# Optimization experiments

Hardware: AMD Instinct MI355X
Metric: run time of the kernel (lower is better)

The kernel has to match this reference:

```python
import jax, jax.numpy as jnp
import numpy as np

COS_EPS = 1e-6
LN_EPS = 1e-5

def _cosine_sim(a, b):
    # PyTorch F.cosine_similarity(dim=1, eps): dot / (max(||a||,eps)*max(||b||,eps))
    dot = jnp.sum(a * b, axis=1)
    na = jnp.maximum(jnp.linalg.norm(a, axis=1), COS_EPS)
    nb = jnp.maximum(jnp.linalg.norm(b, axis=1), COS_EPS)
    return dot / (na * nb)

def _layer_norm(x, gamma, beta):
    mu = jnp.mean(x, axis=-1, keepdims=True)
    var = jnp.mean(jnp.square(x - mu), axis=-1, keepdims=True)
    return (x - mu) * jax.lax.rsqrt(var + LN_EPS) * gamma + beta

def setup_inputs() -> dict:
    B, I, H = 8192, 1024, 1024
    key = jax.random.key(0)
    ks = jax.random.split(key, 10)
    s_in = 1.0 / np.sqrt(I + H)
    s_im = 1.0 / np.sqrt(I)
    return {
        "x": jax.random.normal(ks[0], (B, I), jnp.float32),
        "hx": jax.random.normal(ks[1], (B, H), jnp.float32),
        "cx": jax.random.normal(ks[2], (B, H), jnp.float32),
        # main gate linear: [I+H, 4H]
        "W": jax.random.uniform(ks[3], (I + H, 4 * H), jnp.float32, -s_in, s_in),
        "b": jax.random.uniform(ks[4], (4 * H,), jnp.float32, -s_in, s_in),
        # input_mapped: [I, H]
        "Wm": jax.random.uniform(ks[5], (I, H), jnp.float32, -s_im, s_im),
        "bm": jax.random.uniform(ks[6], (H,), jnp.float32, -s_im, s_im),
        # 4 LayerNorms (i, f, g, o)
        "gammas": 1.0 + 0.1 * jax.random.normal(ks[7], (4, H), jnp.float32),
        "betas": 0.1 * jax.random.normal(ks[8], (4, H), jnp.float32),
    }

def reference(x, hx, cx, W, b, Wm, bm, gammas, betas):
    H = hx.shape[1]
    # cosine attention gate between mapped input and hidden state
    input_mapped = x @ Wm + bm                                   # [B, H]
    attn = jax.nn.sigmoid(_cosine_sim(input_mapped, hx))[:, None]  # [B, 1]
    x_mod = x + attn * x
    gates = jnp.concatenate([x_mod, hx], axis=1) @ W + b         # [B, 4H]
    i_g, f_g, g_g, o_g = jnp.split(gates, 4, axis=1)
    i_g = jax.nn.sigmoid(_layer_norm(i_g, gammas[0], betas[0]))
    f_g = jax.nn.sigmoid(_layer_norm(f_g, gammas[1], betas[1]))
    g_g = jnp.tanh(_layer_norm(g_g, gammas[2], betas[2]))
    o_g = jax.nn.sigmoid(_layer_norm(o_g, gammas[3], betas[3]))
    cx_new = f_g * cx + i_g * g_g
    hx_new = o_g * jnp.tanh(cx_new)
    gate_co = jax.nn.sigmoid((_cosine_sim(hx_new, cx_new)[:, None] + 1.0) / 2.0)
    hx_modulated = hx_new + hx_new * gate_co
    return (hx_modulated, cx_new)
```

## Files before the change

### kernel.cpp

```cpp
#include <hip/hip_runtime.h>
#include <hip/hip_bf16.h>

#define DEV __device__ __forceinline__

typedef unsigned short u16;
typedef unsigned int u32;
typedef __attribute__((ext_vector_type(8))) short bf16x8;
typedef __attribute__((ext_vector_type(4))) float f32x4;

DEV float bf2f(u16 v) { u32 u = ((u32)v) << 16; return __builtin_bit_cast(float, u); }
DEV u16 f2bf(float f) {
    u32 u = __builtin_bit_cast(u32, f);
    u32 r = (u + 0x7fffu + ((u >> 16) & 1u)) >> 16;
    return (u16)r;
}
DEV float lo16(u32 u) { return __builtin_bit_cast(float, u << 16); }
DEV float hi16(u32 u) { return __builtin_bit_cast(float, u & 0xffff0000u); }
DEV float sigm(float x) { return 1.f / (1.f + __expf(-x)); }
DEV float clamp4(float v) { return fminf(fmaxf(v, -1e4f), 1e4f); }
DEV float loadf(const void* p, size_t i, int isf) {
    return isf ? clamp4(((const float*)p)[i]) : clamp4(bf2f(((const u16*)p)[i]));
}
DEV void load8(const void* p, size_t off, int isf, float* o) {
    if (isf) {
        const float* s = (const float*)p + off;
#pragma unroll
        for (int e = 0; e < 8; ++e) o[e] = clamp4(s[e]);
    } else {
        uint4 q = *(const uint4*)((const u16*)p + off);
        o[0] = clamp4(lo16(q.x)); o[1] = clamp4(hi16(q.x));
        o[2] = clamp4(lo16(q.y)); o[3] = clamp4(hi16(q.y));
        o[4] = clamp4(lo16(q.z)); o[5] = clamp4(hi16(q.z));
        o[6] = clamp4(lo16(q.w)); o[7] = clamp4(hi16(q.w));
    }
}
DEV uint4 pack8(const float* a) {
    uint4 q;
    q.x = (u32)f2bf(a[0]) | ((u32)f2bf(a[1]) << 16);
    q.y = (u32)f2bf(a[2]) | ((u32)f2bf(a[3]) << 16);
    q.z = (u32)f2bf(a[4]) | ((u32)f2bf(a[5]) << 16);
    q.w = (u32)f2bf(a[6]) | ((u32)f2bf(a[7]) << 16);
    return q;
}
DEV void store8(void* p, size_t off, int isf, const float* a) {
    if (isf) {
        float* d = (float*)p + off;
        *(float4*)(d) = (float4){a[0], a[1], a[2], a[3]};
        *(float4*)(d + 4) = (float4){a[4], a[5], a[6], a[7]};
    } else {
        *(uint4*)((u16*)p + off) = pack8(a);
    }
}

DEV void gload16(const void* g, void* l) {
    __builtin_amdgcn_global_load_lds(
        (const __attribute__((address_space(1))) void*)g,
        (__attribute__((address_space(3))) void*)l, 16, 0, 0);
}

__global__ void detect_dtype(const u32* __restrict__ xw, u32* __restrict__ flag) {
    const int lane = threadIdx.x & 63;
    int cnt = 0;
    for (int k = 0; k < 32; ++k) {
        u32 e = (xw[lane + 64 * k] >> 7) & 0xff;
        cnt += (e >= 118 && e <= 130) ? 1 : 0;
    }
#pragma unroll
    for (int off = 32; off > 0; off >>= 1) cnt += __shfl_xor(cnt, off, 64);
    if (lane == 0) *flag = (cnt > 1024) ? 0u : 1u;
}

__global__ __launch_bounds__(256) void cvt2_bf16(
    const void* __restrict__ sa, const void* __restrict__ sb,
    u16* __restrict__ da, u16* __restrict__ db, int n8each,
    const u32* __restrict__ flagp) {
    const int isf = (int)*flagp;
    if (!isf) return;
    int i = blockIdx.x * 256 + threadIdx.x;
    const void* s; u16* d; int j;
    if (i < n8each) { s = sa; d = da; j = i; }
    else            { s = sb; d = db; j = i - n8each; }
    size_t off = (size_t)j * 8;
    float a[8];
    load8(s, off, 1, a);
    *(uint4*)(d + off) = pack8(a);
}

__global__ __launch_bounds__(256) void tr_any(const void* __restrict__ src,
                                              u16* __restrict__ dst,
                                              int R, int C,
                                              const u32* __restrict__ flagp) {
    const int isf = (int)*flagp;
    __shared__ __align__(16) u16 t[32][33];
    int tx = threadIdx.x & 31, ty = threadIdx.x >> 5;
    int c0 = blockIdx.x * 32, r0 = blockIdx.y * 32;
#pragma unroll
    for (int i = 0; i < 32; i += 8)
        t[ty + i][tx] = f2bf(loadf(src, (size_t)(r0 + ty + i) * C + (c0 + tx), isf));
    __syncthreads();
#pragma unroll
    for (int i = 0; i < 32; i += 8)
        dst[(size_t)(c0 + ty + i) * R + (r0 + tx)] = t[tx][ty + i];
}

__global__ __launch_bounds__(512, 2) void gemm256(
    const u16* __restrict__ A0c, const void* __restrict__ A0r,
    const u16* __restrict__ A1c, const void* __restrict__ A1r, int K0,
    const u16* __restrict__ Bt, const void* __restrict__ bias,
    const u32* __restrict__ flagp,
    u16* __restrict__ Cout, int M, int N, int K) {
    const int isf = (int)*flagp;
    const u16* const A0 = isf ? A0c : (const u16*)A0r;
    const u16* const A1 = isf ? A1c : (const u16*)A1r;
    __shared__ __align__(16) u16 lds[65536];
    u16* const ldsA = lds;
    u16* const ldsB = lds + 32768;
    const int tid = threadIdx.x;
    const int wave = tid >> 6, lane = tid & 63;
    const int wm = wave >> 2, wn = wave & 3;

    int bx = blockIdx.x, by = blockIdx.y;
    {
        const int gx = gridDim.x;
        const int nwg = gx * gridDim.y;
        if ((nwg & 7) == 0) {
            int lid = by * gx + bx;
            int swz = (lid & 7) * (nwg >> 3) + (lid >> 3);
            bx = swz % gx; by = swz / gx;
        }
    }
    const int m0 = by * 256, n0 = bx * 256;
    const int NT = K >> 6;

    size_t qA[2][2], qB[2][2];
#pragma unroll
    for (int h = 0; h < 2; ++h)
#pragma unroll
        for (int c = 0; c < 2; ++c) {
            int p = h * 16384 + c * 8192 + wave * 1024 + lane * 16;
            int lg = p ^ (((p >> 9) & 1) << 5);
            int s = lg >> 10, lr = (lg >> 6) & 15;
            int k = ((s & 1) << 5) + ((lg & 63) >> 1);
            int m = ((s >> 3) & 1) * 128 + ((s >> 4) & 1) * 64 +
                    ((s >> 1) & 3) * 16 + lr;
            qA[h][c] = (size_t)(m0 + m) * (size_t)K0 + (size_t)k;
            int ns = ((s >> 2) & 3) * 64 + ((s >> 4) & 1) * 32 +
                     ((s >> 1) & 1) * 16 + lr;
            int gn = (ns & ~63) | ((ns & 15) * 4 + ((ns >> 4) & 3));
            qB[h][c] = (size_t)(n0 + gn) * (size_t)K + (size_t)k;
        }

    const int mrow = lane & 15;
    const int kfr = (lane >> 4) * 8;
    const int aSwz = (mrow * 32 + kfr) ^ ((mrow & 8) << 1);

    f32x4 acc[8][4];
#pragma unroll
    for (int i = 0; i < 8; ++i)
#pragma unroll
        for (int j = 0; j < 4; ++j) acc[i][j] = (f32x4){0.f, 0.f, 0.f, 0.f};

#define ASEG(kt, AS_, KK_) const u16* AS_; int KK_; \
    if ((kt) < K0) { AS_ = A0; KK_ = (kt); } else { AS_ = A1; KK_ = (kt) - K0; }

    {
        ASEG(0, As0, kk0);
        gload16(As0 + qA[0][0] + kk0, ldsA + wave * 512);
        gload16(As0 + qA[0][1] + kk0, ldsA + 4096 + wave * 512);
        gload16(Bt + qB[1][0], ldsB + 8192 + wave * 512);
        gload16(Bt + qB[1][1], ldsB + 8192 + 4096 + wave * 512);
        gload16(As0 + qA[1][0] + kk0, ldsA + 8192 + wave * 512);
        gload16(As0 + qA[1][1] + kk0, ldsA + 8192 + 4096 + wave * 512);
        gload16(Bt + qB[0][0], ldsB + wave * 512);
        gload16(Bt + qB[0][1], ldsB + 4096 + wave * 512);
        if (NT > 1) {
            ASEG(64, As1, kk1);
            gload16(As1 + qA[0][0] + kk1, ldsA + 16384 + wave * 512);
            gload16(As1 + qA[0][1] + kk1, ldsA + 16384 + 4096 + wave * 512);
            gload16(Bt + qB[1][0] + 64, ldsB + 16384 + 8192 + wave * 512);
            gload16(Bt + qB[1][1] + 64, ldsB + 16384 + 8192 + 4096 + wave * 512);
            gload16(As1 + qA[1][0] + kk1, ldsA + 16384 + 8192 + wave * 512);
            gload16(As1 + qA[1][1] + kk1, ldsA + 16384 + 8192 + 4096 + wave * 512);
            asm volatile("s_waitcnt vmcnt(6)" ::: "memory");
        } else {
            asm volatile("s_waitcnt vmcnt(0)" ::: "memory");
        }
        __builtin_amdgcn_s_barrier();
    }

    bf16x8 af0[4][2], af1[4][2], bfA[2][2], bfB[2][2];
    {
        const u16* ab = &ldsA[(wm * 8) * 512];
#pragma unroll
        for (int mt2 = 0; mt2 < 4; ++mt2)
#pragma unroll
            for (int ks = 0; ks < 2; ++ks)
                af0[mt2][ks] = *(const bf16x8*)&ab[(mt2 * 2 + ks) * 512 + aSwz];
        const u16* bb = &ldsB[(wn * 4) * 512];
#pragma unroll
        for (int nt2 = 0; nt2 < 2; ++nt2)
#pragma unroll
            for (int ks = 0; ks < 2; ++ks)
                bfA[nt2][ks] = *(const bf16x8*)&bb[(nt2 * 2 + ks) * 512 + aSwz];
    }

    for (int t = 0; t < NT; ++t) {
        const int bufb = (t & 1) << 14;
        const int obufb = bufb ^ 16384;
        const int k0 = t << 6;

        {
            const u16* ab = &ldsA[bufb + (16 + wm * 8) * 512];
#pragma unroll
            for (int mt2 = 0; mt2 < 4; ++mt2)
#pragma unroll
                for (int ks = 0; ks < 2; ++ks)
                    af1[mt2][ks] = *(const bf16x8*)&ab[(mt2 * 2 + ks) * 512 + aSwz];
        }
        if (t + 1 < NT) {
            gload16(Bt + qB[0][0] + (k0 + 64), ldsB + obufb + wave * 512);
            gload16(Bt + qB[0][1] + (k0 + 64), ldsB + obufb + 4096 + wave * 512);
        }
        __builtin_amdgcn_s_barrier();
        __builtin_amdgcn_s_setprio(1);
#pragma unroll
        for (int mt2 = 0; mt2 < 4; ++mt2)
#pragma unroll
            for (int nt2 = 0; nt2 < 2; ++nt2)
#pragma unroll
                for (int ks = 0; ks < 2; ++ks)
                    acc[mt2][nt2] = __builtin_amdgcn_mfma_f32_16x16x32_bf16(
                        af0[mt2][ks], bfA[nt2][ks], acc[mt2][nt2], 0, 0, 0);
        __builtin_amdgcn_s_setprio(0);

        {
            const u16* bb = &ldsB[bufb + (16 + wn * 4) * 512];
#pragma unroll
            for (int nt2 = 0; nt2 < 2; ++nt2)
#pragma unroll
                for (int ks = 0; ks < 2; ++ks)
                    bfB[nt2][ks] = *(const bf16x8*)&bb[(nt2 * 2 + ks) * 512 + aSwz];
        }
        __builtin_amdgcn_s_barrier();
        if (t + 2 < NT) {
            ASEG(k0 + 128, As2, kk2);
            gload16(As2 + qA[0][0] + kk2, ldsA + bufb + wave * 512);
            gload16(As2 + qA[0][1] + kk2, ldsA + bufb + 4096 + wave * 512);
        }
        __builtin_amdgcn_s_setprio(1);
#pragma unroll
        for (int mt2 = 0; mt2 < 4; ++mt2)
#pragma unroll
            for (int nt2 = 0; nt2 < 2; ++nt2)
#pragma unroll
                for (int ks = 0; ks < 2; ++ks)
                    acc[4 + mt2][nt2] = __builtin_amdgcn_mfma_f32_16x16x32_bf16(
                        af1[mt2][ks], bfA[nt2][ks], acc[4 + mt2][nt2], 0, 0, 0);
#pragma unroll
        for (int mt2 = 0; mt2 < 4; ++mt2)
#pragma unroll
            for (int nt2 = 0; nt2 < 2; ++nt2)
#pragma unroll
                for (int ks = 0; ks < 2; ++ks)
                    acc[mt2][2 + nt2] = __builtin_amdgcn_mfma_f32_16x16x32_bf16(
                        af0[mt2][ks], bfB[nt2][ks], acc[mt2][2 + nt2], 0, 0, 0);
        __builtin_amdgcn_s_setprio(0);

        __builtin_amdgcn_s_barrier();
        if (t + 2 < NT) {
            gload16(Bt + qB[1][0] + (k0 + 128), ldsB + bufb + 8192 + wave * 512);
            gload16(Bt + qB[1][1] + (k0 + 128), ldsB + bufb + 8192 + 4096 + wave * 512);
            ASEG(k0 + 128, As3, kk3);
            gload16(As3 + qA[1][0] + kk3, ldsA + bufb + 8192 + wave * 512);
            gload16(As3 + qA[1][1] + kk3, ldsA + bufb + 8192 + 4096 + wave * 512);
            asm volatile("s_waitcnt vmcnt(6)" ::: "memory");
        } else {
            asm volatile("s_waitcnt vmcnt(0)" ::: "memory");
        }
        __builtin_amdgcn_s_barrier();
        if (t + 1 < NT) {
            const u16* ab = &ldsA[obufb + (wm * 8) * 512];
#pragma unroll
            for (int mt2 = 0; mt2 < 4; ++mt2)
#pragma unroll
                for (int ks = 0; ks < 2; ++ks)
                    af0[mt2][ks] = *(const bf16x8*)&ab[(mt2 * 2 + ks) * 512 + aSwz];
            const u16* bb = &ldsB[obufb + (wn * 4) * 512];
#pragma unroll
            for (int nt2 = 0; nt2 < 2; ++nt2)
#pragma unroll
                for (int ks = 0; ks < 2; ++ks)
                    bfA[nt2][ks] = *(const bf16x8*)&bb[(nt2 * 2 + ks) * 512 + aSwz];
        }
        __builtin_amdgcn_s_setprio(1);
#pragma unroll
        for (int mt2 = 0; mt2 < 4; ++mt2)
#pragma unroll
            for (int nt2 = 0; nt2 < 2; ++nt2)
#pragma unroll
                for (int ks = 0; ks < 2; ++ks)
                    acc[4 + mt2][2 + nt2] = __builtin_amdgcn_mfma_f32_16x16x32_bf16(
                        af1[mt2][ks], bfB[nt2][ks], acc[4 + mt2][2 + nt2], 0, 0, 0);
        __builtin_amdgcn_s_setprio(0);
    }
#undef ASEG

    const int q = lane >> 4;
    const int cbase = n0 + wn * 64 + mrow * 4;
    float bv[4];
#pragma unroll
    for (int tt = 0; tt < 4; ++tt) bv[tt] = loadf(bias, cbase + tt, isf);
#pragma unroll
    for (int mt = 0; mt < 8; ++mt) {
        int row0 = m0 + wm * 128 + mt * 16 + q * 4;
#pragma unroll
        for (int r = 0; r < 4; ++r) {
            uint2 pk;
            pk.x = (u32)f2bf(acc[mt][0][r] + bv[0]) |
                   ((u32)f2bf(acc[mt][1][r] + bv[1]) << 16);
            pk.y = (u32)f2bf(acc[mt][2][r] + bv[2]) |
                   ((u32)f2bf(acc[mt][3][r] + bv[3]) << 16);
            *(uint2*)(Cout + (size_t)(row0 + r) * N + cbase) = pk;
        }
    }
}

__global__ __launch_bounds__(256) void attn_xmod(
    const u16* __restrict__ im,
    const u16* __restrict__ hxc, const void* __restrict__ hxr,
    const u16* __restrict__ xc, const void* __restrict__ xr,
    const u32* __restrict__ flagp, u16* __restrict__ xmod) {
    const int isf = (int)*flagp;
    const u16* hx = isf ? hxc : (const u16*)hxr;
    const u16* x = isf ? xc : (const u16*)xr;
    const int lane = threadIdx.x & 63;
    const int row = blockIdx.x * 4 + (threadIdx.x >> 6);
    float dot = 0.f, na = 0.f, nb = 0.f;
#pragma unroll
    for (int j = 0; j < 2; ++j) {
        size_t off = (size_t)row * 1024 + lane * 8 + j * 512;
        float a[8], h[8];
        load8(im, off, 0, a);
        load8(hx, off, 0, h);
#pragma unroll
        for (int e = 0; e < 8; ++e) {
            dot += a[e] * h[e]; na += a[e] * a[e]; nb += h[e] * h[e];
        }
    }
#pragma unroll
    for (int off = 32; off > 0; off >>= 1) {
        dot += __shfl_xor(dot, off, 64);
        na += __shfl_xor(na, off, 64);
        nb += __shfl_xor(nb, off, 64);
    }
    float cs = dot / (fmaxf(sqrtf(na), 1e-6f) * fmaxf(sqrtf(nb), 1e-6f));
    float fac = 1.f + sigm(cs);
#pragma unroll
    for (int j = 0; j < 2; ++j) {
        size_t off = (size_t)row * 1024 + lane * 8 + j * 512;
        float a[8];
        load8(x, off, 0, a);
#pragma unroll
        for (int e = 0; e < 8; ++e) a[e] *= fac;
        *(uint4*)(xmod + off) = pack8(a);
    }
}

__global__ __launch_bounds__(256) void ln_lstm(
    const u16* __restrict__ gates, const void* __restrict__ cx,
    const void* __restrict__ gammas, const void* __restrict__ betas,
    const u32* __restrict__ flagp, void* __restrict__ out, int BH) {
    const int isf = (int)*flagp;
    const int lane = threadIdx.x & 63;
    const int row = blockIdx.x * 4 + (threadIdx.x >> 6);
    float v[4][16];
    float s[4] = {0.f, 0.f, 0.f, 0.f}, ss[4] = {0.f, 0.f, 0.f, 0.f};
#pragma unroll
    for (int c = 0; c < 4; ++c) {
#pragma unroll
        for (int j = 0; j < 2; ++j) {
            size_t off = (size_t)row * 4096 + c * 1024 + lane * 8 + j * 512;
            float* vp = &v[c][j * 8];
            load8(gates, off, 0, vp);
#pragma unroll
            for (int e = 0; e < 8; ++e) { s[c] += vp[e]; ss[c] += vp[e] * vp[e]; }
        }
    }
#pragma unroll
    for (int off = 32; off > 0; off >>= 1) {
#pragma unroll
        for (int c = 0; c < 4; ++c) {
            s[c] += __shfl_xor(s[c], off, 64);
            ss[c] += __shfl_xor(ss[c], off, 64);
        }
    }
    float mean[4], rstd[4];
#pragma unroll
    for (int c = 0; c < 4; ++c) {
        mean[c] = s[c] * (1.f / 1024.f);
        float var = ss[c] * (1.f / 1024.f) - mean[c] * mean[c];
        rstd[c] = rsqrtf(fmaxf(var, 0.f) + 1e-5f);
    }
#pragma unroll
    for (int c = 0; c < 4; ++c) {
#pragma unroll
        for (int j = 0; j < 2; ++j) {
            size_t off = (size_t)(c * 1024 + lane * 8 + j * 512);
            float g[8], bb[8];
            load8(gammas, off, isf, g);
            load8(betas, off, isf, bb);
            float* vp = &v[c][j * 8];
#pragma unroll
            for (int e = 0; e < 8; ++e) {
                float y = (vp[e] - mean[c]) * rstd[c] * g[e] + bb[e];
                vp[e] = (c == 2) ? tanhf(y) : sigm(y);
            }
        }
    }
    float hn[16], cn[16];
    float dot = 0.f, nh = 0.f, nc = 0.f;
#pragma unroll
    for (int j = 0; j < 2; ++j) {
        size_t off = (size_t)row * 1024 + lane * 8 + j * 512;
        float cv[8];
        load8(cx, off, isf, cv);
#pragma unroll
        for (int e = 0; e < 8; ++e) {
            int idx = j * 8 + e;
            float c_new = v[1][idx] * cv[e] + v[0][idx] * v[2][idx];
            float h_new = v[3][idx] * tanhf(c_new);
            cn[idx] = c_new; hn[idx] = h_new;
            dot += h_new * c_new; nh += h_new * h_new; nc += c_new * c_new;
        }
    }
#pragma unroll
    for (int off = 32; off > 0; off >>= 1) {
        dot += __shfl_xor(dot, off, 64);
        nh += __shfl_xor(nh, off, 64);
        nc += __shfl_xor(nc, off, 64);
    }
    float cs = dot / (fmaxf(sqrtf(nh), 1e-6f) * fmaxf(sqrtf(nc), 1e-6f));
    float fac = 1.f + sigm((cs + 1.f) * 0.5f);
#pragma unroll
    for (int j = 0; j < 2; ++j) {
        size_t off = (size_t)row * 1024 + lane * 8 + j * 512;
        float ho[8];
#pragma unroll
        for (int e = 0; e < 8; ++e) ho[e] = hn[j * 8 + e] * fac;
        store8(out, off, isf, ho);
        store8(out, (size_t)BH + off, isf, &cn[j * 8]);
    }
}

__global__ void diag_k(u32* __restrict__ out, int ws_ok, int sizes_ok) {
    const int lane = threadIdx.x & 63;
    int mrow = lane & 15, quad = lane >> 4;
    bf16x8 af, bfr;
#pragma unroll
    for (int j = 0; j < 8; ++j) {
        int k = quad * 8 + j;
        af[j] = (short)f2bf((float)(((mrow * 7 + k * 3) % 11) - 5));
        bfr[j] = (short)f2bf((float)(((mrow * 5 + k * 2) % 13) - 6));
    }
    f32x4 cacc = (f32x4){0.f, 0.f, 0.f, 0.f};
    cacc = __builtin_amdgcn_mfma_f32_16x16x32_bf16(af, bfr, cacc, 0, 0, 0);
    int bad = 0;
#pragma unroll
    for (int r = 0; r < 4; ++r) {
        int mr = quad * 4 + r;
        float expv = 0.f;
        for (int k = 0; k < 32; ++k)
            expv += (float)(((mr * 7 + k * 3) % 11) - 5) *
                    (float)(((mrow * 5 + k * 2) % 13) - 6);
        if (fabsf(cacc[r] - expv) > 0.5f) bad = 1;
    }
    int mfma_bad = (__ballot(bad) != 0ull) ? 1 : 0;
    if (lane == 0) {
        if (!sizes_ok)     out[0] = __builtin_bit_cast(u32, 65536.f);
        else if (!ws_ok)   out[0] = __builtin_bit_cast(u32, 131072.f);
        else if (mfma_bad) out[0] = __builtin_bit_cast(u32, 32768.f);
    }
}

extern "C" void kernel_launch(void* const* d_in, const int* in_sizes, int n_in,
                              void* d_out, int out_size, void* d_ws, size_t ws_size,
                              hipStream_t stream) {
    const void* x   = d_in[0];
    const void* hx  = d_in[1];
    const void* cx  = d_in[2];
    const void* W   = d_in[3];
    const void* b   = d_in[4];
    const void* Wm  = d_in[5];
    const void* bm  = d_in[6];
    const void* gam = d_in[7];
    const void* bet = d_in[8];

    const int B = 8192, I = 1024, H = 1024;
    const int K2 = I + H, N2 = 4 * H;
    const size_t MiB = 1048576ull;

    char* ws = (char*)d_ws;
    u16* x_c   = (u16*)ws;
    u16* hx_c  = (u16*)(ws + 16 * MiB);
    u16* Wt    = (u16*)(ws + 32 * MiB);
    u16* Wmt   = (u16*)(ws + 48 * MiB);
    u16* gates = (u16*)(ws + 50 * MiB);
    u32* flag  = (u32*)(ws + 114 * MiB);
    u16* xmod  = (u16*)d_out;
    u16* imb   = (u16*)d_out + 8388608ull;

    const int sizes_ok =
        n_in == 9 && out_size == 16777216 &&
        in_sizes[0] == 8388608 && in_sizes[1] == 8388608 && in_sizes[2] == 8388608 &&
        in_sizes[3] == 8388608 && in_sizes[4] == 4096 && in_sizes[5] == 1048576 &&
        in_sizes[6] == 1024 && in_sizes[7] == 4096 && in_sizes[8] == 4096;
    const int ws_ok = ws_size >= 115 * MiB;

    if (sizes_ok && ws_ok) {
        detect_dtype<<<1, 64, 0, stream>>>((const u32*)x, flag);
        cvt2_bf16<<<8192, 256, 0, stream>>>(x, hx, x_c, hx_c, 1048576, flag);
        tr_any<<<dim3(H / 32, I / 32), 256, 0, stream>>>(Wm, Wmt, I, H, flag);
        tr_any<<<dim3(N2 / 32, K2 / 32), 256, 0, stream>>>(W, Wt, K2, N2, flag);
        gemm256<<<dim3(H / 256, B / 256), 512, 0, stream>>>(
            x_c, x, x_c, x, I, Wmt, bm, flag, imb, B, H, I);
        attn_xmod<<<dim3(B / 4), 256, 0, stream>>>(imb, hx_c, hx, x_c, x, flag, xmod);
        gemm256<<<dim3(N2 / 256, B / 256), 512, 0, stream>>>(
            xmod, xmod, hx_c, hx, I, Wt, b, flag, gates, B, N2, K2);
        ln_lstm<<<dim3(B / 4), 256, 0, stream>>>(gates, cx, gam, bet, flag,
                                                 d_out, B * H);
    }
    diag_k<<<1, 64, 0, stream>>>((u32*)d_out, ws_ok, sizes_ok);
}
```

Measured before the change: 411.3 us.

## Restructure GEMM main loop into barrier-gated four-phase ping-pong schedule

```diff
diff --git a/kernel.cpp b/kernel.cpp
--- a/kernel.cpp
+++ b/kernel.cpp
@@ -56,6 +56,17 @@
     __builtin_amdgcn_global_load_lds(
         (const __attribute__((address_space(1))) void*)g,
         (__attribute__((address_space(3))) void*)l, 16, 0, 0);
+}
+
+DEV void phase_gate() {
+    __builtin_amdgcn_s_barrier();
+    asm volatile("s_waitcnt lgkmcnt(0)" ::: "memory");
+    __builtin_amdgcn_sched_barrier(0);
+    __builtin_amdgcn_s_setprio(1);
+}
+DEV void phase_close() {
+    __builtin_amdgcn_s_setprio(0);
+    __builtin_amdgcn_s_barrier();
 }
 
 __global__ void detect_dtype(const u32* __restrict__ xw, u32* __restrict__ flag) {
@@ -163,147 +174,124 @@
 #define ASEG(kt, AS_, KK_) const u16* AS_; int KK_; \
     if ((kt) < K0) { AS_ = A0; KK_ = (kt); } else { AS_ = A1; KK_ = (kt) - K0; }
 
+#define RD_A(dst, off16) { const u16* ab_ = &ldsA[off16]; \
+    _Pragma("unroll") for (int mt2 = 0; mt2 < 4; ++mt2) \
+    _Pragma("unroll") for (int ks = 0; ks < 2; ++ks) \
+        dst[mt2][ks] = *(const bf16x8*)&ab_[(mt2 * 2 + ks) * 512 + aSwz]; }
+
+#define RD_B(dst, off16) { const u16* bb_ = &ldsB[off16]; \
+    _Pragma("unroll") for (int nt2 = 0; nt2 < 2; ++nt2) \
+    _Pragma("unroll") for (int ks = 0; ks < 2; ++ks) \
+        dst[nt2][ks] = *(const bf16x8*)&bb_[(nt2 * 2 + ks) * 512 + aSwz]; }
+
+#define MFMA_Q(AF, BF, MO, NO) \
+    _Pragma("unroll") for (int mt2 = 0; mt2 < 4; ++mt2) \
+    _Pragma("unroll") for (int nt2 = 0; nt2 < 2; ++nt2) \
+    _Pragma("unroll") for (int ks = 0; ks < 2; ++ks) \
+        acc[(MO) + mt2][(NO) + nt2] = __builtin_amdgcn_mfma_f32_16x16x32_bf16( \
+            AF[mt2][ks], BF[nt2][ks], acc[(MO) + mt2][(NO) + nt2], 0, 0, 0);
+
     {
-        ASEG(0, As0, kk0);
-        gload16(As0 + qA[0][0] + kk0, ldsA + wave * 512);
-        gload16(As0 + qA[0][1] + kk0, ldsA + 4096 + wave * 512);
+        { ASEG(0, As_, kk_);
+          gload16(As_ + qA[0][0] + kk_, ldsA + wave * 512);
+          gload16(As_ + qA[0][1] + kk_, ldsA + 4096 + wave * 512); }
         gload16(Bt + qB[1][0], ldsB + 8192 + wave * 512);
         gload16(Bt + qB[1][1], ldsB + 8192 + 4096 + wave * 512);
-        gload16(As0 + qA[1][0] + kk0, ldsA + 8192 + wave * 512);
-        gload16(As0 + qA[1][1] + kk0, ldsA + 8192 + 4096 + wave * 512);
+        { ASEG(0, As_, kk_);
+          gload16(As_ + qA[1][0] + kk_, ldsA + 8192 + wave * 512);
+          gload16(As_ + qA[1][1] + kk_, ldsA + 8192 + 4096 + wave * 512); }
         gload16(Bt + qB[0][0], ldsB + wave * 512);
         gload16(Bt + qB[0][1], ldsB + 4096 + wave * 512);
-        if (NT > 1) {
-            ASEG(64, As1, kk1);
-            gload16(As1 + qA[0][0] + kk1, ldsA + 16384 + wave * 512);
-            gload16(As1 + qA[0][1] + kk1, ldsA + 16384 + 4096 + wave * 512);
-            gload16(Bt + qB[1][0] + 64, ldsB + 16384 + 8192 + wave * 512);
-            gload16(Bt + qB[1][1] + 64, ldsB + 16384 + 8192 + 4096 + wave * 512);
-            gload16(As1 + qA[1][0] + kk1, ldsA + 16384 + 8192 + wave * 512);
-            gload16(As1 + qA[1][1] + kk1, ldsA + 16384 + 8192 + 4096 + wave * 512);
-            asm volatile("s_waitcnt vmcnt(6)" ::: "memory");
-        } else {
-            asm volatile("s_waitcnt vmcnt(0)" ::: "memory");
-        }
+        { ASEG(64, As_, kk_);
+          gload16(As_ + qA[0][0] + kk_, ldsA + 16384 + wave * 512);
+          gload16(As_ + qA[0][1] + kk_, ldsA + 16384 + 4096 + wave * 512); }
+        gload16(Bt + qB[1][0] + 64, ldsB + 16384 + 8192 + wave * 512);
+        gload16(Bt + qB[1][1] + 64, ldsB + 16384 + 8192 + 4096 + wave * 512);
+        { ASEG(64, As_, kk_);
+          gload16(As_ + qA[1][0] + kk_, ldsA + 16384 + 8192 + wave * 512);
+          gload16(As_ + qA[1][1] + kk_, ldsA + 16384 + 8192 + 4096 + wave * 512); }
+        asm volatile("s_waitcnt vmcnt(6)" ::: "memory");
         __builtin_amdgcn_s_barrier();
     }
 
     bf16x8 af0[4][2], af1[4][2], bfA[2][2], bfB[2][2];
-    {
-        const u16* ab = &ldsA[(wm * 8) * 512];
-#pragma unroll
-        for (int mt2 = 0; mt2 < 4; ++mt2)
-#pragma unroll
-            for (int ks = 0; ks < 2; ++ks)
-                af0[mt2][ks] = *(const bf16x8*)&ab[(mt2 * 2 + ks) * 512 + aSwz];
-        const u16* bb = &ldsB[(wn * 4) * 512];
-#pragma unroll
-        for (int nt2 = 0; nt2 < 2; ++nt2)
-#pragma unroll
-            for (int ks = 0; ks < 2; ++ks)
-                bfA[nt2][ks] = *(const bf16x8*)&bb[(nt2 * 2 + ks) * 512 + aSwz];
-    }
-
-    for (int t = 0; t < NT; ++t) {
-        const int bufb = (t & 1) << 14;
-        const int obufb = bufb ^ 16384;
-        const int k0 = t << 6;
-
-        {
-            const u16* ab = &ldsA[bufb + (16 + wm * 8) * 512];
-#pragma unroll
-            for (int mt2 = 0; mt2 < 4; ++mt2)
-#pragma unroll
-                for (int ks = 0; ks < 2; ++ks)
-                    af1[mt2][ks] = *(const bf16x8*)&ab[(mt2 * 2 + ks) * 512 + aSwz];
-        }
-        if (t + 1 < NT) {
-            gload16(Bt + qB[0][0] + (k0 + 64), ldsB + obufb + wave * 512);
-            gload16(Bt + qB[0][1] + (k0 + 64), ldsB + obufb + 4096 + wave * 512);
-        }
+    for (int t = 0; t < NT; t += 2) {
+        const bool more = (t + 2) < NT;
+        const int kt1 = (t + 1) << 6, kt2 = (t + 2) << 6, kt3 = (t + 3) << 6;
+
+        RD_A(af0, (wm * 8) * 512);
+        RD_B(bfA, (wn * 4) * 512);
+        gload16(Bt + qB[0][0] + kt1, ldsB + 16384 + wave * 512);
+        gload16(Bt + qB[0][1] + kt1, ldsB + 16384 + 4096 + wave * 512);
+        phase_gate();
+        MFMA_Q(af0, bfA, 0, 0);
+        phase_close();
+
+        RD_B(bfB, (16 + wn * 4) * 512);
+        if (more) { ASEG(kt2, As_, kk_);
+            gload16(As_ + qA[0][0] + kk_, ldsA + wave * 512);
+            gload16(As_ + qA[0][1] + kk_, ldsA + 4096 + wave * 512); }
+        phase_gate();
+        MFMA_Q(af0, bfB, 0, 2);
+        phase_close();
+
+        RD_A(af1, (16 + wm * 8) * 512);
+        if (more) {
+            gload16(Bt + qB[1][0] + kt2, ldsB + 8192 + wave * 512);
+            gload16(Bt + qB[1][1] + kt2, ldsB + 8192 + 4096 + wave * 512); }
+        phase_gate();
+        MFMA_Q(af1, bfB, 4, 2);
+        phase_close();
+
+        if (more) { ASEG(kt2, As_, kk_);
+            gload16(As_ + qA[1][0] + kk_, ldsA + 8192 + wave * 512);
+            gload16(As_ + qA[1][1] + kk_, ldsA + 8192 + 4096 + wave * 512); }
+        phase_gate();
+        MFMA_Q(af1, bfA, 4, 0);
+        __builtin_amdgcn_s_setprio(0);
+        if (more) asm volatile("s_waitcnt vmcnt(6)" ::: "memory");
+        else      asm volatile("s_waitcnt vmcnt(0)" ::: "memory");
         __builtin_amdgcn_s_barrier();
-        __builtin_amdgcn_s_setprio(1);
-#pragma unroll
-        for (int mt2 = 0; mt2 < 4; ++mt2)
-#pragma unroll
-            for (int nt2 = 0; nt2 < 2; ++nt2)
-#pragma unroll
-                for (int ks = 0; ks < 2; ++ks)
-                    acc[mt2][nt2] = __builtin_amdgcn_mfma_f32_16x16x32_bf16(
-                        af0[mt2][ks], bfA[nt2][ks], acc[mt2][nt2], 0, 0, 0);
+
+        RD_A(af0, 16384 + (wm * 8) * 512);
+        RD_B(bfA, 16384 + (wn * 4) * 512);
+        if (more) {
+            gload16(Bt + qB[0][0] + kt2, ldsB + wave * 512);
+            gload16(Bt + qB[0][1] + kt2, ldsB + 4096 + wave * 512); }
+        phase_gate();
+        MFMA_Q(af0, bfA, 0, 0);
+        phase_close();
+
+        RD_B(bfB, 16384 + (16 + wn * 4) * 512);
+        if (more) { ASEG(kt3, As_, kk_);
+            gload16(As_ + qA[0][0] + kk_, ldsA + 16384 + wave * 512);
+            gload16(As_ + qA[0][1] + kk_, ldsA + 16384 + 4096 + wave * 512); }
+        phase_gate();
+        MFMA_Q(af0, bfB, 0, 2);
+        phase_close();
+
+        RD_A(af1, 16384 + (16 + wm * 8) * 512);
+        if (more) {
+            gload16(Bt + qB[1][0] + kt3, ldsB + 16384 + 8192 + wave * 512);
+            gload16(Bt + qB[1][1] + kt3, ldsB + 16384 + 8192 + 4096 + wave * 512); }
+        phase_gate();
+        MFMA_Q(af1, bfB, 4, 2);
+        phase_close();
+
+        if (more) { ASEG(kt3, As_, kk_);
+            gload16(As_ + qA[1][0] + kk_, ldsA + 16384 + 8192 + wave * 512);
+            gload16(As_ + qA[1][1] + kk_, ldsA + 16384 + 8192 + 4096 + wave * 512); }
+        phase_gate();
+        MFMA_Q(af1, bfA, 4, 0);
         __builtin_amdgcn_s_setprio(0);
-
-        {
-            const u16* bb = &ldsB[bufb + (16 + wn * 4) * 512];
-#pragma unroll
-            for (int nt2 = 0; nt2 < 2; ++nt2)
-#pragma unroll
-                for (int ks = 0; ks < 2; ++ks)
-                    bfB[nt2][ks] = *(const bf16x8*)&bb[(nt2 * 2 + ks) * 512 + aSwz];
-        }
+        if (more) asm volatile("s_waitcnt vmcnt(6)" ::: "memory");
+        else      asm volatile("s_waitcnt vmcnt(0)" ::: "memory");
         __builtin_amdgcn_s_barrier();
-        if (t + 2 < NT) {
-            ASEG(k0 + 128, As2, kk2);
-            gload16(As2 + qA[0][0] + kk2, ldsA + bufb + wave * 512);
-            gload16(As2 + qA[0][1] + kk2, ldsA + bufb + 4096 + wave * 512);
-        }
-        __builtin_amdgcn_s_setprio(1);
-#pragma unroll
-        for (int mt2 = 0; mt2 < 4; ++mt2)
-#pragma unroll
-            for (int nt2 = 0; nt2 < 2; ++nt2)
-#pragma unroll
-                for (int ks = 0; ks < 2; ++ks)
-                    acc[4 + mt2][nt2] = __builtin_amdgcn_mfma_f32_16x16x32_bf16(
-                        af1[mt2][ks], bfA[nt2][ks], acc[4 + mt2][nt2], 0, 0, 0);
-#pragma unroll
-        for (int mt2 = 0; mt2 < 4; ++mt2)
-#pragma unroll
-            for (int nt2 = 0; nt2 < 2; ++nt2)
-#pragma unroll
-                for (int ks = 0; ks < 2; ++ks)
-                    acc[mt2][2 + nt2] = __builtin_amdgcn_mfma_f32_16x16x32_bf16(
-                        af0[mt2][ks], bfB[nt2][ks], acc[mt2][2 + nt2], 0, 0, 0);
-        __builtin_amdgcn_s_setprio(0);
-
-        __builtin_amdgcn_s_barrier();
-        if (t + 2 < NT) {
-            gload16(Bt + qB[1][0] + (k0 + 128), ldsB + bufb + 8192 + wave * 512);
-            gload16(Bt + qB[1][1] + (k0 + 128), ldsB + bufb + 8192 + 4096 + wave * 512);
-            ASEG(k0 + 128, As3, kk3);
-            gload16(As3 + qA[1][0] + kk3, ldsA + bufb + 8192 + wave * 512);
-            gload16(As3 + qA[1][1] + kk3, ldsA + bufb + 8192 + 4096 + wave * 512);
-            asm volatile("s_waitcnt vmcnt(6)" ::: "memory");
-        } else {
-            asm volatile("s_waitcnt vmcnt(0)" ::: "memory");
-        }
-        __builtin_amdgcn_s_barrier();
-        if (t + 1 < NT) {
-            const u16* ab = &ldsA[obufb + (wm * 8) * 512];
-#pragma unroll
-            for (int mt2 = 0; mt2 < 4; ++mt2)
-#pragma unroll
-                for (int ks = 0; ks < 2; ++ks)
-                    af0[mt2][ks] = *(const bf16x8*)&ab[(mt2 * 2 + ks) * 512 + aSwz];
-            const u16* bb = &ldsB[obufb + (wn * 4) * 512];
-#pragma unroll
-            for (int nt2 = 0; nt2 < 2; ++nt2)
-#pragma unroll
-                for (int ks = 0; ks < 2; ++ks)
-                    bfA[nt2][ks] = *(const bf16x8*)&bb[(nt2 * 2 + ks) * 512 + aSwz];
-        }
-        __builtin_amdgcn_s_setprio(1);
-#pragma unroll
-        for (int mt2 = 0; mt2 < 4; ++mt2)
-#pragma unroll
-            for (int nt2 = 0; nt2 < 2; ++nt2)
-#pragma unroll
-                for (int ks = 0; ks < 2; ++ks)
-                    acc[4 + mt2][2 + nt2] = __builtin_amdgcn_mfma_f32_16x16x32_bf16(
-                        af1[mt2][ks], bfB[nt2][ks], acc[4 + mt2][2 + nt2], 0, 0, 0);
-        __builtin_amdgcn_s_setprio(0);
     }
 #undef ASEG
+#undef RD_A
+#undef RD_B
+#undef MFMA_Q
 
     const int q = lane >> 4;
     const int cbase = n0 + wn * 64 + mrow * 4;
```

Result: no change. 416.8 us (+1.3%).
